# Performance work log

Measured on AMD Instinct MI355X. Metric: run time of the kernel, lower is better.

The kernel has to match this reference:

```python
import jax, jax.numpy as jnp
import numpy as np

B, S, DIM = 2, 2048, 2048
H, KV = 16, 8
HD = DIM // H          # 128 head_dim
N_REP = H // KV        # 2


def _rope(x, cos, sin):
    # x: (B,S,h,HD) with interleaved (real, imag) pairs along last dim
    xr = x[..., 0::2]                      # (B,S,h,HD/2)
    xi = x[..., 1::2]
    cos = cos[None, :, None, :]            # (1,S,1,HD/2)
    sin = sin[None, :, None, :]
    or_ = xr * cos - xi * sin
    oi_ = xr * sin + xi * cos
    return jnp.stack([or_, oi_], axis=-1).reshape(x.shape)


def setup_inputs() -> dict:
    key = jax.random.key(0)
    ks = jax.random.split(key, 5)
    x = jax.random.normal(ks[0], (B, S, DIM), dtype=jnp.float32)
    # RoPE tables: theta = 10000, half = HD/2
    inv_freq = 1.0 / (10000.0 ** (np.arange(0, HD, 2, dtype=np.float32) / HD))
    t = np.arange(S, dtype=np.float32)
    ang = np.outer(t, inv_freq)                           # (S, HD/2)
    freqs_cos = jnp.asarray(np.cos(ang), dtype=jnp.float32)
    freqs_sin = jnp.asarray(np.sin(ang), dtype=jnp.float32)
    sc = 0.02
    wq = jax.random.normal(ks[1], (DIM, H * HD), dtype=jnp.float32) * sc
    wk = jax.random.normal(ks[2], (DIM, KV * HD), dtype=jnp.float32) * sc
    wv = jax.random.normal(ks[3], (DIM, KV * HD), dtype=jnp.float32) * sc
    wo = jax.random.normal(ks[4], (DIM, DIM), dtype=jnp.float32) * sc
    return {"x": x, "freqs_cos": freqs_cos, "freqs_sin": freqs_sin,
            "wq": wq, "wk": wk, "wv": wv, "wo": wo}


def reference(x, freqs_cos, freqs_sin, wq, wk, wv, wo):
    b, s, _ = x.shape
    xq = (x @ wq).reshape(b, s, H, HD)
    xk = (x @ wk).reshape(b, s, KV, HD)
    xv = (x @ wv).reshape(b, s, KV, HD)
    xq = _rope(xq, freqs_cos, freqs_sin)
    xk = _rope(xk, freqs_cos, freqs_sin)
    # GQA: repeat kv heads n_rep times along head axis
    xk = jnp.repeat(xk, N_REP, axis=2)     # (b,s,H,HD)
    xv = jnp.repeat(xv, N_REP, axis=2)
    scores = jnp.einsum('bqhd,bkhd->bhqk', xq, xk) / jnp.sqrt(
        jnp.asarray(HD, dtype=x.dtype))
    mask = jnp.triu(jnp.full((s, s), -jnp.inf, dtype=x.dtype), k=1)
    attn = jax.nn.softmax(scores + mask[None, None, :, :], axis=-1)
    out = jnp.einsum('bhqk,bkhd->bqhd', attn, xv).reshape(b, s, DIM)
    return out @ wo
```

## Files before the change

### kernel.cpp

```cpp
#include <hip/hip_runtime.h>

typedef unsigned short u16;
typedef short bf16x8 __attribute__((ext_vector_type(8)));
typedef float f32x4 __attribute__((ext_vector_type(4)));
typedef unsigned int u32x4 __attribute__((ext_vector_type(4)));
typedef unsigned short u16x4 __attribute__((ext_vector_type(4)));
typedef unsigned short u16x8 __attribute__((ext_vector_type(8)));

#define S_LEN 2048
#define NHEAD 16
#define NKV 8
#define HD 128

__device__ __forceinline__ u16 f2bf(float f) {
  unsigned u = __builtin_bit_cast(unsigned, f);
  u = (u + 0x7FFFu + ((u >> 16) & 1u)) >> 16;
  return (u16)u;
}
__device__ __forceinline__ float bf2f(u16 h) {
  unsigned u = ((unsigned)h) << 16;
  return __builtin_bit_cast(float, u);
}

__device__ __forceinline__ void gl_lds16(const void* g, void* l) {
  __builtin_amdgcn_global_load_lds(
      (const __attribute__((address_space(1))) unsigned int*)g,
      (__attribute__((address_space(3))) unsigned int*)l, 16, 0, 0);
}

__device__ __forceinline__ float redmax16(float v) {
  v = fmaxf(v, __shfl_xor(v, 1));
  v = fmaxf(v, __shfl_xor(v, 2));
  v = fmaxf(v, __shfl_xor(v, 4));
  v = fmaxf(v, __shfl_xor(v, 8));
  return v;
}

__global__ __launch_bounds__(256) void conv_bf16(const float* __restrict__ in,
                                                 u16* __restrict__ out, int n4) {
  int i = blockIdx.x * 256 + threadIdx.x;
  if (i >= n4) return;
  f32x4 v = *(const f32x4*)(in + (size_t)i * 4);
  u16x4 o;
#pragma unroll
  for (int j = 0; j < 4; ++j) o[j] = f2bf(v[j]);
  *(u16x4*)(out + (size_t)i * 4) = o;
}

__global__ __launch_bounds__(256) void transpose_w4(
    const float* __restrict__ wq, const float* __restrict__ wk,
    const float* __restrict__ wv, const float* __restrict__ wo,
    u16* __restrict__ wcatT, u16* __restrict__ woT) {
  __shared__ float tile[64][65];
  int id = blockIdx.x;
  const float* in;
  u16* out;
  int N, roff, nx;
  if (id < 1024) {
    in = wq; out = wcatT; N = 2048; roff = 0; nx = 32;
  } else if (id < 1536) {
    in = wk; out = wcatT; N = 1024; roff = 2048; nx = 16; id -= 1024;
  } else if (id < 2048) {
    in = wv; out = wcatT; N = 1024; roff = 3072; nx = 16; id -= 1536;
  } else {
    in = wo; out = woT; N = 2048; roff = 0; nx = 32; id -= 2048;
  }
  int bx = id % nx;
  int by = id / nx;
  int k0 = by * 64, n0 = bx * 64;
  int tx = threadIdx.x & 63, ty = threadIdx.x >> 6;
#pragma unroll
  for (int p = 0; p < 16; ++p) {
    int r = p * 4 + ty;
    tile[r][tx] = in[(size_t)(k0 + r) * N + n0 + tx];
  }
  __syncthreads();
#pragma unroll
  for (int p = 0; p < 16; ++p) {
    int r = p * 4 + ty;
    out[(size_t)(roff + n0 + r) * 2048 + k0 + tx] = f2bf(tile[tx][r]);
  }
}

__global__ __launch_bounds__(256) void rope_qk(u16* __restrict__ q, u16* __restrict__ k,
                                               const float* __restrict__ fc,
                                               const float* __restrict__ fs) {
  const int QC = 2 * NHEAD * S_LEN * HD / 8;
  const int KC = 2 * NKV * S_LEN * HD / 8;
  int i = blockIdx.x * 256 + threadIdx.x;
  if (i >= QC + KC) return;
  u16* base;
  float scale;
  size_t e;
  if (i < QC) {
    base = q;
    e = (size_t)i * 8;
    scale = 0.12751744540368598f;
  } else {
    base = k;
    e = (size_t)(i - QC) * 8;
    scale = 1.0f;
  }
  int d8 = (int)(e & 127);
  int s = (int)((e >> 7) & (S_LEN - 1));
  int dp0 = d8 >> 1;
  u16x8 v = *(const u16x8*)(base + e);
  u16x8 o;
#pragma unroll
  for (int p = 0; p < 4; ++p) {
    float xr = bf2f(v[2 * p]), xi = bf2f(v[2 * p + 1]);
    float c = fc[s * 64 + dp0 + p], sn = fs[s * 64 + dp0 + p];
    o[2 * p] = f2bf((xr * c - xi * sn) * scale);
    o[2 * p + 1] = f2bf((xr * sn + xi * c) * scale);
  }
  *(u16x8*)(base + e) = o;
}

template <int EPI, int BM>
__global__ __launch_bounds__(512, 2) void gemm8(
    const u16* __restrict__ A, const u16* __restrict__ Bt, float* __restrict__ Cf,
    u16* __restrict__ Qo, u16* __restrict__ Ko, u16* __restrict__ Vo, int N, int ntn) {
  constexpr int K = 2048, NT = K / 32;
  constexpr int ASZ = BM * 32, TSZ = ASZ + 256 * 32;
  constexpr int L = (BM + 256) / 128;
  __shared__ __align__(16) u16 lds[4][TSZ];

  const int t = threadIdx.x;
  const int l = t & 63, lh = l >> 4, ll = l & 15;
  const int w = t >> 6, wm = w >> 2, wn = w & 3;

  const int bid = blockIdx.x;
  const int swz = (bid & 7) * (gridDim.x >> 3) + (bid >> 3);
  const int tm = swz / ntn, tn = swz % ntn;

  const u16* Ab = A + (size_t)tm * BM * K;
  const u16* Bb = Bt + (size_t)tn * 256 * K;

  const int sr = t >> 2;
  const int sc8 = ((t & 3) ^ (sr & 3)) * 8;
  const int cb = (lh ^ (ll & 3)) * 8;

  f32x4 acc[BM / 32][4] = {};

  auto STAGE = [&](int tau) {
    const int kt = tau * 32;
    u16* buf = &lds[tau & 3][0];
#pragma unroll
    for (int c = 0; c < BM / 128; ++c)
      gl_lds16(Ab + (size_t)(c * 128 + sr) * K + kt + sc8, buf + c * 4096 + t * 8);
#pragma unroll
    for (int c = 0; c < 2; ++c)
      gl_lds16(Bb + (size_t)(c * 128 + sr) * K + kt + sc8, buf + ASZ + c * 4096 + t * 8);
  };

  STAGE(0);
  STAGE(1);
  STAGE(2);
  __builtin_amdgcn_s_waitcnt(0xF70 | (2 * L));
  __builtin_amdgcn_s_barrier();
  asm volatile("" ::: "memory");

  for (int tt = 0; tt < NT; ++tt) {
    if (tt + 3 < NT) STAGE(tt + 3);
    const u16* buf = &lds[tt & 3][0];
#pragma unroll
    for (int ph = 0; ph < BM / 128; ++ph) {
      bf16x8 af[4], bv[4];
#pragma unroll
      for (int i = 0; i < 4; ++i)
        af[i] =
            *(const bf16x8*)(buf + (wm * (BM / 2) + (ph * 4 + i) * 16 + ll) * 32 + cb);
#pragma unroll
      for (int n = 0; n < 4; ++n)
        bv[n] = *(const bf16x8*)(buf + ASZ + (wn * 64 + n * 16 + ll) * 32 + cb);
      __builtin_amdgcn_s_setprio(1);
#pragma unroll
      for (int i = 0; i < 4; ++i)
#pragma unroll
        for (int n = 0; n < 4; ++n)
          acc[ph * 4 + i][n] = __builtin_amdgcn_mfma_f32_16x16x32_bf16(
              af[i], bv[n], acc[ph * 4 + i][n], 0, 0, 0);
      __builtin_amdgcn_s_setprio(0);
    }
    if (tt + 1 < NT) {
      if (tt + 3 < NT)
        __builtin_amdgcn_s_waitcnt(0xF70 | (2 * L));
      else if (tt + 2 < NT)
        __builtin_amdgcn_s_waitcnt(0xF70 | L);
      else
        __builtin_amdgcn_s_waitcnt(0xF70);
      __builtin_amdgcn_s_barrier();
      asm volatile("" ::: "memory");
    }
  }

#pragma unroll
  for (int m = 0; m < BM / 32; ++m)
#pragma unroll
    for (int n = 0; n < 4; ++n)
#pragma unroll
      for (int j = 0; j < 4; ++j) {
        int row = tm * BM + wm * (BM / 2) + m * 16 + lh * 4 + j;
        int col = tn * 256 + wn * 64 + n * 16 + ll;
        if constexpr (EPI == 0) {
          Cf[(size_t)row * N + col] = acc[m][n][j];
        } else {
          int b = row >> 11, s = row & (S_LEN - 1);
          u16 val = f2bf(acc[m][n][j]);
          int d = col & 127;
          if (col < 2048) {
            int hh = col >> 7;
            Qo[(((size_t)b * NHEAD + hh) * S_LEN + s) * HD + d] = val;
          } else if (col < 3072) {
            int kh = (col >> 7) & 7;
            Ko[(((size_t)b * NKV + kh) * S_LEN + s) * HD + d] = val;
          } else {
            int kh = (col >> 7) & 7;
            Vo[(((size_t)b * NKV + kh) * S_LEN + s) * HD + d] = val;
          }
        }
      }
}

__global__ __launch_bounds__(256) void transpose_v(const u16* __restrict__ V,
                                                   u16* __restrict__ Vt) {
  __shared__ u16 tile[64][72];
  int id = blockIdx.x;
  int bkv = id >> 6;
  int dt = (id >> 5) & 1;
  int st = id & 31;
  const u16* Vb = V + (size_t)bkv * S_LEN * HD;
  u16* Vo = Vt + (size_t)bkv * HD * S_LEN;
  int r = threadIdx.x >> 3, c8 = (threadIdx.x & 7) * 8;
#pragma unroll
  for (int it = 0; it < 2; ++it) {
    int rr = it * 32 + r;
    *(u16x8*)(&tile[rr][c8]) =
        *(const u16x8*)(Vb + (size_t)(st * 64 + rr) * HD + dt * 64 + c8);
  }
  __syncthreads();
#pragma unroll
  for (int it = 0; it < 2; ++it) {
    int rr = it * 32 + r;
    u16x8 o;
#pragma unroll
    for (int j = 0; j < 8; ++j) o[j] = tile[c8 + j][rr];
    *(u16x8*)(Vo + (size_t)(dt * 64 + rr) * S_LEN + st * 64 + c8) = o;
  }
}

__global__ __launch_bounds__(256) void attn_fwd(const u16* __restrict__ Q,
                                                const u16* __restrict__ Kh,
                                                const u16* __restrict__ Vt,
                                                u16* __restrict__ O) {
  __shared__ __align__(16) u16 Ks[64 * 136];
  __shared__ __align__(16) u16 Vs[128 * 72];
  __shared__ __align__(16) u16 Ps[4 * 16 * 64];

  const int t = threadIdx.x;
  const int w = t >> 6, l = t & 63, lh = l >> 4, ll = l & 15;
  const int bid = blockIdx.x;
  const int swzb = (bid & 7) * 64 + (bid >> 3);
  const int bh = swzb >> 4;
  const int pair = swzb & 15;
  const int b = bh >> 4, h = bh & 15;
  const int bkv = b * NKV + (h >> 1);

  const u16* Qb = Q + (size_t)bh * S_LEN * HD;
  const u16* Kb = Kh + (size_t)bkv * S_LEN * HD;
  const u16* Vb = Vt + (size_t)bkv * HD * S_LEN;

  const int krow = t >> 4, kcol = (t & 15) * 8;
  const int vrow = t >> 3, vcol = (t & 7) * 8;

  const bf16x8 vones = {0x3F80, 0x3F80, 0x3F80, 0x3F80, 0x3F80, 0x3F80, 0x3F80, 0x3F80};

  auto loadKV = [&](int tile, u32x4 (&kr)[4], u32x4 (&vr)[4]) {
    const int kv0 = tile * 64;
#pragma unroll
    for (int p = 0; p < 4; ++p)
      kr[p] = *(const u32x4*)(Kb + (size_t)(kv0 + p * 16 + krow) * HD + kcol);
#pragma unroll
    for (int p = 0; p < 4; ++p)
      vr[p] = *(const u32x4*)(Vb + (size_t)(p * 32 + vrow) * S_LEN + kv0 + vcol);
  };
  auto storeKV = [&](u32x4 (&kr)[4], u32x4 (&vr)[4]) {
#pragma unroll
    for (int p = 0; p < 4; ++p)
      *(u32x4*)(Ks + (p * 16 + krow) * 136 + kcol) = kr[p];
#pragma unroll
    for (int p = 0; p < 4; ++p)
      *(u32x4*)(Vs + (p * 32 + vrow) * 72 + vcol) = vr[p];
  };

  for (int hf = 0; hf < 2; ++hf) {
    const int qt = hf ? (31 - pair) : pair;
    const int q0 = qt * 64;

    bf16x8 qf[4];
    const int qrow = q0 + w * 16 + ll;
#pragma unroll
    for (int c = 0; c < 4; ++c)
      qf[c] = *(const bf16x8*)(Qb + (size_t)qrow * HD + c * 32 + lh * 8);

    f32x4 accO[8] = {};
    f32x4 accL = {0.f, 0.f, 0.f, 0.f};
    float mrow[4] = {-1e30f, -1e30f, -1e30f, -1e30f};

    u32x4 kr[4], vr[4];
    loadKV(0, kr, vr);
    storeKV(kr, vr);
    __syncthreads();

    const int nt = qt + 1;
    for (int tt = 0; tt < nt; ++tt) {
      if (tt + 1 < nt) loadKV(tt + 1, kr, vr);

      f32x4 sf[4];
#pragma unroll
      for (int f = 0; f < 4; ++f) {
        sf[f] = f32x4{0.f, 0.f, 0.f, 0.f};
#pragma unroll
        for (int c = 0; c < 4; ++c) {
          bf16x8 kf = *(const bf16x8*)(Ks + (f * 16 + ll) * 136 + c * 32 + lh * 8);
          sf[f] = __builtin_amdgcn_mfma_f32_16x16x32_bf16(qf[c], kf, sf[f], 0, 0, 0);
        }
      }

      if (tt == nt - 1) {
        const int kv0 = tt * 64;
#pragma unroll
        for (int f = 0; f < 4; ++f)
#pragma unroll
          for (int j = 0; j < 4; ++j) {
            int kvg = kv0 + f * 16 + ll;
            int qg = q0 + w * 16 + lh * 4 + j;
            if (kvg > qg) sf[f][j] = -1e30f;
          }
      }

      float corr[4];
#pragma unroll
      for (int j = 0; j < 4; ++j) {
        float mx = fmaxf(fmaxf(sf[0][j], sf[1][j]), fmaxf(sf[2][j], sf[3][j]));
        mx = redmax16(mx);
        float mnew = fmaxf(mrow[j], mx);
        corr[j] = __builtin_amdgcn_exp2f(mrow[j] - mnew);
        mrow[j] = mnew;
#pragma unroll
        for (int f = 0; f < 4; ++f) sf[f][j] = __builtin_amdgcn_exp2f(sf[f][j] - mnew);
      }
#pragma unroll
      for (int n = 0; n < 8; ++n)
#pragma unroll
        for (int j = 0; j < 4; ++j) accO[n][j] *= corr[j];
#pragma unroll
      for (int j = 0; j < 4; ++j) accL[j] *= corr[j];

      char* Pw = (char*)(Ps + w * 16 * 64);
#pragma unroll
      for (int f = 0; f < 4; ++f)
#pragma unroll
        for (int j = 0; j < 4; ++j) {
          int rr = lh * 4 + j, cc = f * 16 + ll;
          unsigned bo = (unsigned)(rr * 128 + cc * 2) ^ (unsigned)((rr & 7) << 4);
          *(u16*)(Pw + bo) = f2bf(sf[f][j]);
        }

#pragma unroll
      for (int kc = 0; kc < 2; ++kc) {
        unsigned bo =
            (unsigned)(ll * 128 + (kc * 32 + lh * 8) * 2) ^ (unsigned)((ll & 7) << 4);
        bf16x8 pf = *(const bf16x8*)(Pw + bo);
#pragma unroll
        for (int n = 0; n < 8; ++n) {
          bf16x8 vf = *(const bf16x8*)(Vs + (n * 16 + ll) * 72 + kc * 32 + lh * 8);
          accO[n] = __builtin_amdgcn_mfma_f32_16x16x32_bf16(pf, vf, accO[n], 0, 0, 0);
        }
        accL = __builtin_amdgcn_mfma_f32_16x16x32_bf16(pf, vones, accL, 0, 0, 0);
      }

      __syncthreads();
      if (tt + 1 < nt) storeKV(kr, vr);
      __syncthreads();
    }

    float inv[4];
#pragma unroll
    for (int j = 0; j < 4; ++j) inv[j] = 1.0f / accL[j];
    const size_t orow = (size_t)(b * S_LEN + q0 + w * 16 + lh * 4) * 2048 + h * HD;
#pragma unroll
    for (int n = 0; n < 8; ++n)
#pragma unroll
      for (int j = 0; j < 4; ++j)
        O[orow + (size_t)j * 2048 + n * 16 + ll] = f2bf(accO[n][j] * inv[j]);
  }
}

extern "C" void kernel_launch(void* const* d_in, const int* in_sizes, int n_in,
                              void* d_out, int out_size, void* d_ws, size_t ws_size,
                              hipStream_t stream) {
  (void)in_sizes;
  (void)n_in;
  (void)out_size;
  (void)ws_size;
  const float* x = (const float*)d_in[0];
  const float* fc = (const float*)d_in[1];
  const float* fs = (const float*)d_in[2];
  const float* wq = (const float*)d_in[3];
  const float* wk = (const float*)d_in[4];
  const float* wv = (const float*)d_in[5];
  const float* wo = (const float*)d_in[6];
  float* out = (float*)d_out;

  char* ws = (char*)d_ws;
  u16* wcatT = (u16*)ws;
  u16* vtb = (u16*)ws;
  u16* woT = (u16*)(ws + 16777216);
  u16* xo = (u16*)(ws + 25165824);
  u16* qb = (u16*)(ws + 41943040);
  u16* kb = (u16*)(ws + 58720256);
  u16* vb = (u16*)(ws + 67108864);

  conv_bf16<<<8192, 256, 0, stream>>>(x, xo, 2097152);
  transpose_w4<<<3072, 256, 0, stream>>>(wq, wk, wv, wo, wcatT, woT);

  gemm8<1, 256><<<256, 512, 0, stream>>>(xo, wcatT, nullptr, qb, kb, vb, 4096, 16);
  transpose_v<<<1024, 256, 0, stream>>>(vb, vtb);
  rope_qk<<<6144, 256, 0, stream>>>(qb, kb, fc, fs);
  attn_fwd<<<512, 256, 0, stream>>>(qb, kb, vtb, xo);
  gemm8<0, 128><<<256, 512, 0, stream>>>(xo, woT, out, nullptr, nullptr, nullptr, 2048,
                                         8);
}
```

Baseline: 234.4 us.

## Replace GEMM with 128x256 tile, K=64 steps, triple-buffered LDS

Replaces the templated GEMM with a fixed 128x256 output tile that advances K in steps of 64 and keeps three LDS buffers with prefetch distance two instead of four buffers at distance three. The XOR swizzle is widened to 8 chunks to match the 64-wide rows. Launch bounds drop to one block per SM because LDS use grows, and the QKV GEMM launches 512 blocks of the smaller M tile instead of 256. The aim is fewer barriers per K and a better grid fill for the QKV projection, at the cost of less B-tile reuse and lower occupancy.

New measurement: 233.3 us. No clear change (-0.4%).

```diff
diff --git a/kernel.cpp b/kernel.cpp
--- a/kernel.cpp
+++ b/kernel.cpp
@@ -116,14 +116,13 @@
   *(u16x8*)(base + e) = o;
 }
 
-template <int EPI, int BM>
-__global__ __launch_bounds__(512, 2) void gemm8(
+template <int EPI>
+__global__ __launch_bounds__(512, 1) void gemm3r(
     const u16* __restrict__ A, const u16* __restrict__ Bt, float* __restrict__ Cf,
     u16* __restrict__ Qo, u16* __restrict__ Ko, u16* __restrict__ Vo, int N, int ntn) {
-  constexpr int K = 2048, NT = K / 32;
-  constexpr int ASZ = BM * 32, TSZ = ASZ + 256 * 32;
-  constexpr int L = (BM + 256) / 128;
-  __shared__ __align__(16) u16 lds[4][TSZ];
+  constexpr int K = 2048, NT = K / 64;
+  constexpr int BSZ = (128 + 256) * 64;
+  __shared__ __align__(16) u16 lds[3][BSZ];
 
   const int t = threadIdx.x;
   const int l = t & 63, lh = l >> 4, ll = l & 15;
@@ -133,60 +132,58 @@
   const int swz = (bid & 7) * (gridDim.x >> 3) + (bid >> 3);
   const int tm = swz / ntn, tn = swz % ntn;
 
-  const u16* Ab = A + (size_t)tm * BM * K;
+  const u16* Ab = A + (size_t)tm * 128 * K;
   const u16* Bb = Bt + (size_t)tn * 256 * K;
 
-  const int sr = t >> 2;
-  const int sc8 = ((t & 3) ^ (sr & 3)) * 8;
-  const int cb = (lh ^ (ll & 3)) * 8;
-
-  f32x4 acc[BM / 32][4] = {};
+  const int sr = t >> 3;
+  const int sc8 = ((t & 7) ^ (sr & 7)) * 8;
+
+  f32x4 acc[4][4] = {};
 
   auto STAGE = [&](int tau) {
-    const int kt = tau * 32;
-    u16* buf = &lds[tau & 3][0];
-#pragma unroll
-    for (int c = 0; c < BM / 128; ++c)
-      gl_lds16(Ab + (size_t)(c * 128 + sr) * K + kt + sc8, buf + c * 4096 + t * 8);
+    const int kt = tau * 64;
+    u16* buf = &lds[tau % 3][0];
 #pragma unroll
     for (int c = 0; c < 2; ++c)
-      gl_lds16(Bb + (size_t)(c * 128 + sr) * K + kt + sc8, buf + ASZ + c * 4096 + t * 8);
+      gl_lds16(Ab + (size_t)(c * 64 + sr) * K + kt + sc8, buf + c * 4096 + t * 8);
+#pragma unroll
+    for (int c = 0; c < 4; ++c)
+      gl_lds16(Bb + (size_t)(c * 64 + sr) * K + kt + sc8,
+               buf + 8192 + c * 4096 + t * 8);
   };
 
   STAGE(0);
   STAGE(1);
-  STAGE(2);
-  __builtin_amdgcn_s_waitcnt(0xF70 | (2 * L));
+  __builtin_amdgcn_s_waitcnt(0xF70 | 6);
   __builtin_amdgcn_s_barrier();
   asm volatile("" ::: "memory");
 
   for (int tt = 0; tt < NT; ++tt) {
-    if (tt + 3 < NT) STAGE(tt + 3);
-    const u16* buf = &lds[tt & 3][0];
-#pragma unroll
-    for (int ph = 0; ph < BM / 128; ++ph) {
+    if (tt + 2 < NT) STAGE(tt + 2);
+    const u16* bufA = &lds[tt % 3][0];
+    const u16* bufB = bufA + 8192;
+#pragma unroll
+    for (int kk = 0; kk < 2; ++kk) {
+      const int cb = ((kk * 4 + lh) ^ (ll & 7)) * 8;
       bf16x8 af[4], bv[4];
 #pragma unroll
-      for (int i = 0; i < 4; ++i)
-        af[i] =
-            *(const bf16x8*)(buf + (wm * (BM / 2) + (ph * 4 + i) * 16 + ll) * 32 + cb);
+      for (int m = 0; m < 4; ++m)
+        af[m] = *(const bf16x8*)(bufA + (wm * 64 + m * 16 + ll) * 64 + cb);
 #pragma unroll
       for (int n = 0; n < 4; ++n)
-        bv[n] = *(const bf16x8*)(buf + ASZ + (wn * 64 + n * 16 + ll) * 32 + cb);
+        bv[n] = *(const bf16x8*)(bufB + (wn * 64 + n * 16 + ll) * 64 + cb);
       __builtin_amdgcn_s_setprio(1);
 #pragma unroll
-      for (int i = 0; i < 4; ++i)
+      for (int m = 0; m < 4; ++m)
 #pragma unroll
         for (int n = 0; n < 4; ++n)
-          acc[ph * 4 + i][n] = __builtin_amdgcn_mfma_f32_16x16x32_bf16(
-              af[i], bv[n], acc[ph * 4 + i][n], 0, 0, 0);
+          acc[m][n] =
+              __builtin_amdgcn_mfma_f32_16x16x32_bf16(af[m], bv[n], acc[m][n], 0, 0, 0);
       __builtin_amdgcn_s_setprio(0);
     }
     if (tt + 1 < NT) {
-      if (tt + 3 < NT)
-        __builtin_amdgcn_s_waitcnt(0xF70 | (2 * L));
-      else if (tt + 2 < NT)
-        __builtin_amdgcn_s_waitcnt(0xF70 | L);
+      if (tt + 2 < NT)
+        __builtin_amdgcn_s_waitcnt(0xF70 | 6);
       else
         __builtin_amdgcn_s_waitcnt(0xF70);
       __builtin_amdgcn_s_barrier();
@@ -195,12 +192,12 @@
   }
 
 #pragma unroll
-  for (int m = 0; m < BM / 32; ++m)
+  for (int m = 0; m < 4; ++m)
 #pragma unroll
     for (int n = 0; n < 4; ++n)
 #pragma unroll
       for (int j = 0; j < 4; ++j) {
-        int row = tm * BM + wm * (BM / 2) + m * 16 + lh * 4 + j;
+        int row = tm * 128 + wm * 64 + m * 16 + lh * 4 + j;
         int col = tn * 256 + wn * 64 + n * 16 + ll;
         if constexpr (EPI == 0) {
           Cf[(size_t)row * N + col] = acc[m][n][j];
@@ -425,10 +422,9 @@
   conv_bf16<<<8192, 256, 0, stream>>>(x, xo, 2097152);
   transpose_w4<<<3072, 256, 0, stream>>>(wq, wk, wv, wo, wcatT, woT);
 
-  gemm8<1, 256><<<256, 512, 0, stream>>>(xo, wcatT, nullptr, qb, kb, vb, 4096, 16);
+  gemm3r<1><<<512, 512, 0, stream>>>(xo, wcatT, nullptr, qb, kb, vb, 4096, 16);
   transpose_v<<<1024, 256, 0, stream>>>(vb, vtb);
   rope_qk<<<6144, 256, 0, stream>>>(qb, kb, fc, fs);
   attn_fwd<<<512, 256, 0, stream>>>(qb, kb, vtb, xo);
-  gemm8<0, 128><<<256, 512, 0, stream>>>(xo, woT, out, nullptr, nullptr, nullptr, 2048,
-                                         8);
-}
+  gemm3r<0><<<256, 512, 0, stream>>>(xo, woT, out, nullptr, nullptr, nullptr, 2048, 8);
+}
```
